# Performance work log

Hardware: AMD Instinct MI355X
Metric: run time of the kernel (lower is better)

## Reference

```python
import jax, jax.numpy as jnp
import numpy as np

N, D, DFF, E, K = 16384, 1024, 4096, 8, 2


def setup_inputs() -> dict:
    key = jax.random.key(0)
    ks = jax.random.split(key, 4)
    return {
        "x": jax.random.normal(ks[0], (N, D), jnp.float32),
        "gate_W": jax.random.normal(ks[1], (D, E), jnp.float32) * (D ** -0.5),
        "gate_b": jnp.zeros((E,), jnp.float32),
        "W1": jax.random.normal(ks[2], (E, D, DFF), jnp.float32) * (D ** -0.5),
        "b1": jnp.zeros((E, DFF), jnp.float32),
        "W2": jax.random.normal(ks[3], (E, DFF, D), jnp.float32) * (DFF ** -0.5),
        "b2": jnp.zeros((E, D), jnp.float32),
    }


def reference(x, gate_W, gate_b, W1, b1, W2, b2):
    n = x.shape[0]
    # --- gating: top-k logits -> softmax over the selected k ---
    logits = x @ gate_W + gate_b                      # [N, E]
    top_v, top_i = jax.lax.top_k(logits, K)           # [N, K]
    w = jax.nn.softmax(top_v, axis=1)                 # [N, K]
    # combine weight per (token, expert); tokens not routed to e get 0,
    # reproducing the masked gather + weighted index_add_ of the original.
    comb = jnp.zeros((n, E), x.dtype).at[jnp.arange(n)[:, None], top_i].add(w)  # [N, E]

    out = jnp.zeros((n, W2.shape[-1]), x.dtype)
    for e in range(E):  # small fixed expert count
        h = jax.nn.gelu(x @ W1[e] + b1[e], approximate=False)  # [N, DFF]
        y = h @ W2[e] + b2[e]                                   # [N, D]
        out = out + comb[:, e:e + 1] * y
    return out, top_i
```

## Files before the change

### kernel.cpp

```cpp
#include <hip/hip_runtime.h>
#include <math.h>

#define N_TOK 16384
#define DIM   1024
#define DFF_  4096
#define NE    8
#define MAXTILES 264
#define MAXSLOTS (MAXTILES*128)

typedef __attribute__((ext_vector_type(8))) __bf16 bf16x8;
typedef __attribute__((ext_vector_type(4))) float  f32x4;
typedef __attribute__((ext_vector_type(8))) unsigned short u16x8;

__device__ __forceinline__ unsigned short f2bf(float f) {
    union { float f; unsigned int u; } v; v.f = f;
    unsigned int u = v.u;
    unsigned int r = (u + 0x7fffu + ((u >> 16) & 1u)) >> 16;
    return (unsigned short)r;
}

__device__ __forceinline__ void gl_lds16(const void* g, void* l) {
    __builtin_amdgcn_global_load_lds(
        (const __attribute__((address_space(1))) void*)g,
        (__attribute__((address_space(3))) void*)l, 16, 0, 0);
}

__global__ __launch_bounds__(256)
void conv_x_kernel(const float* __restrict__ in, unsigned short* __restrict__ outp, int n8) {
    for (int i = blockIdx.x * 256 + threadIdx.x; i < n8; i += gridDim.x * 256) {
        const float4* pp = reinterpret_cast<const float4*>(in + (size_t)i * 8);
        float4 a = pp[0], b = pp[1];
        u16x8 o;
        o[0]=f2bf(a.x); o[1]=f2bf(a.y); o[2]=f2bf(a.z); o[3]=f2bf(a.w);
        o[4]=f2bf(b.x); o[5]=f2bf(b.y); o[6]=f2bf(b.z); o[7]=f2bf(b.w);
        *reinterpret_cast<u16x8*>(outp + (size_t)i * 8) = o;
    }
}

__global__ __launch_bounds__(256)
void transpose_conv(const float* __restrict__ in, unsigned short* __restrict__ outp, int R, int C) {
    __shared__ float tile[32][33];
    size_t mat = (size_t)R * C;
    const float* src = in + (size_t)blockIdx.z * mat;
    unsigned short* dst = outp + (size_t)blockIdx.z * mat;
    int c0 = blockIdx.x * 32, r0 = blockIdx.y * 32;
    int tc = threadIdx.x & 31, tr = threadIdx.x >> 5;
#pragma unroll
    for (int i = 0; i < 4; ++i)
        tile[tr + i*8][tc] = src[(size_t)(r0 + tr + i*8) * C + (c0 + tc)];
    __syncthreads();
#pragma unroll
    for (int i = 0; i < 4; ++i) {
        int a = tr + i*8;
        dst[(size_t)(c0 + a) * R + (r0 + tc)] = f2bf(tile[tc][a]);
    }
}

__global__ __launch_bounds__(256)
void gate_kernel(const float* __restrict__ x, const float* __restrict__ gW,
                 const float* __restrict__ gb, float* __restrict__ outIdx,
                 int* __restrict__ tokE, float* __restrict__ tokW, int* __restrict__ counts) {
    int wave = threadIdx.x >> 6, lane = threadIdx.x & 63;
    int tok = blockIdx.x * 4 + wave;
    const float* xr = x + (size_t)tok * DIM;
    float p[NE];
#pragma unroll
    for (int e = 0; e < NE; ++e) p[e] = 0.f;
    for (int i = lane; i < DIM; i += 64) {
        float xi = xr[i];
        const float* g = gW + (size_t)i * NE;
#pragma unroll
        for (int e = 0; e < NE; ++e) p[e] += xi * g[e];
    }
#pragma unroll
    for (int off = 32; off > 0; off >>= 1) {
#pragma unroll
        for (int e = 0; e < NE; ++e) p[e] += __shfl_xor(p[e], off, 64);
    }
    if (lane == 0) {
        float v0 = -1e30f, v1 = -1e30f; int i0 = 0, i1 = 0;
#pragma unroll
        for (int e = 0; e < NE; ++e) {
            float l = p[e] + gb[e];
            if (l > v0)      { v1 = v0; i1 = i0; v0 = l; i0 = e; }
            else if (l > v1) { v1 = l; i1 = e; }
        }
        float e1 = expf(v1 - v0);
        float inv = 1.0f / (1.0f + e1);
        outIdx[tok*2]   = (float)i0;
        outIdx[tok*2+1] = (float)i1;
        tokE[tok*2] = i0; tokE[tok*2+1] = i1;
        tokW[tok*2] = inv; tokW[tok*2+1] = e1 * inv;
        atomicAdd(&counts[i0], 1);
        atomicAdd(&counts[i1], 1);
    }
}

__global__ void offsets_kernel(const int* __restrict__ counts, int* __restrict__ P,
                               int* __restrict__ tileinfo) {
    if (threadIdx.x == 0 && blockIdx.x == 0) {
        int off = 0, tid = 0;
        for (int e = 0; e < NE; ++e) {
            P[e] = off;
            int c = counts[e];
            int nt = (c + 127) >> 7;
            for (int tt = 0; tt < nt; ++tt) {
                tileinfo[tid*4+0] = e;
                tileinfo[tid*4+1] = off + tt*128;
                int v = c - tt*128; if (v > 128) v = 128;
                tileinfo[tid*4+2] = v;
                tid++;
            }
            off += nt << 7;
        }
        for (; tid < MAXTILES; ++tid) tileinfo[tid*4+0] = -1;
    }
}

__global__ __launch_bounds__(256)
void scatter_kernel(const int* __restrict__ tokE, const float* __restrict__ tokW,
                    const int* __restrict__ P, int* __restrict__ cursor,
                    int* __restrict__ rowlist, float* __restrict__ slotW) {
    int tk = blockIdx.x * 256 + threadIdx.x;
    if (tk >= N_TOK) return;
#pragma unroll
    for (int k = 0; k < 2; ++k) {
        int e = tokE[tk*2 + k];
        int pos = atomicAdd(&cursor[e], 1);
        int slot = P[e] + pos;
        rowlist[slot] = tk;
        slotW[slot]  = tokW[tk*2 + k];
    }
}

__global__ __launch_bounds__(256, 2)
void moe_gemm1(const unsigned short* __restrict__ xb,
               const unsigned short* __restrict__ W1t,
               const float* __restrict__ b1,
               const int* __restrict__ tileinfo,
               const int* __restrict__ rowlist,
               unsigned short* __restrict__ h) {
    int rs = blockIdx.x;
    int e = tileinfo[rs*4];
    if (e < 0) return;
    int base   = tileinfo[rs*4+1];
    int nvalid = tileinfo[rs*4+2];
    int colBlk = blockIdx.y;

    __shared__ unsigned short As[128*64];
    __shared__ unsigned short Bs[128*64];

    int t = threadIdx.x;
    int wave = t >> 6, lane = t & 63;
    int wr = wave >> 1, wc = wave & 1;
    int lr = lane >> 3;
    int lk = (lane & 7) * 8;

    const unsigned short* aSrc[4];
    const unsigned short* bSrc[4];
#pragma unroll
    for (int i = 0; i < 4; ++i) {
        int r = i*32 + wave*8 + lr;
        int tok = (r < nvalid) ? rowlist[base + r] : rowlist[base];
        aSrc[i] = xb + (size_t)tok * DIM + lk;
        int cb = colBlk*128 + r;
        bSrc[i] = W1t + (size_t)e * DFF_ * DIM + (size_t)cb * DIM + lk;
    }

    f32x4 acc[4][4] = {};

    for (int kt = 0; kt < DIM/64; ++kt) {
        __syncthreads();
        int ko = kt * 64;
#pragma unroll
        for (int i = 0; i < 4; ++i) {
            gl_lds16(aSrc[i] + ko, &As[(i*32 + wave*8)*64]);
            gl_lds16(bSrc[i] + ko, &Bs[(i*32 + wave*8)*64]);
        }
        __syncthreads();
#pragma unroll
        for (int kk = 0; kk < 2; ++kk) {
            bf16x8 a[4], b[4];
#pragma unroll
            for (int m = 0; m < 4; ++m)
                a[m] = *reinterpret_cast<const bf16x8*>(&As[(wr*64 + m*16 + (lane&15))*64 + kk*32 + (lane>>4)*8]);
#pragma unroll
            for (int n = 0; n < 4; ++n)
                b[n] = *reinterpret_cast<const bf16x8*>(&Bs[(wc*64 + n*16 + (lane&15))*64 + kk*32 + (lane>>4)*8]);
#pragma unroll
            for (int m = 0; m < 4; ++m)
#pragma unroll
                for (int n = 0; n < 4; ++n)
                    acc[m][n] = __builtin_amdgcn_mfma_f32_16x16x32_bf16(a[m], b[n], acc[m][n], 0, 0, 0);
        }
    }

    float bv[4];
#pragma unroll
    for (int n = 0; n < 4; ++n)
        bv[n] = b1[(size_t)e*DFF_ + colBlk*128 + wc*64 + n*16 + (lane & 15)];
#pragma unroll
    for (int m = 0; m < 4; ++m) {
        int rbase = wr*64 + m*16 + (lane>>4)*4;
#pragma unroll
        for (int j = 0; j < 4; ++j) {
            int row = rbase + j;
            size_t hrow = (size_t)(base + row) * DFF_;
#pragma unroll
            for (int n = 0; n < 4; ++n) {
                int col = colBlk*128 + wc*64 + n*16 + (lane & 15);
                unsigned short val;
                if (row < nvalid) {
                    float v = acc[m][n][j] + bv[n];
                    v = 0.5f * v * (1.0f + erff(v * 0.70710678118654752f));
                    val = f2bf(v);
                } else {
                    val = 0;
                }
                h[hrow + col] = val;
            }
        }
    }
}

__global__ __launch_bounds__(256, 2)
void moe_gemm2(const unsigned short* __restrict__ h,
               const unsigned short* __restrict__ W2t,
               const float* __restrict__ b2,
               const int* __restrict__ tileinfo,
               const int* __restrict__ rowlist,
               const float* __restrict__ slotW,
               float* __restrict__ outp) {
    int rs = blockIdx.x;
    int e = tileinfo[rs*4];
    if (e < 0) return;
    int base   = tileinfo[rs*4+1];
    int nvalid = tileinfo[rs*4+2];
    int colBlk = blockIdx.y;

    __shared__ unsigned short As[128*64];
    __shared__ unsigned short Bs[128*64];

    int t = threadIdx.x;
    int wave = t >> 6, lane = t & 63;
    int wr = wave >> 1, wc = wave & 1;
    int lr = lane >> 3;
    int lk = (lane & 7) * 8;

    const unsigned short* aSrc[4];
    const unsigned short* bSrc[4];
#pragma unroll
    for (int i = 0; i < 4; ++i) {
        int r = i*32 + wave*8 + lr;
        aSrc[i] = h + (size_t)(base + r) * DFF_ + lk;
        int cb = colBlk*128 + r;
        bSrc[i] = W2t + (size_t)e * DIM * DFF_ + (size_t)cb * DFF_ + lk;
    }

    f32x4 acc[4][4] = {};

    for (int kt = 0; kt < DFF_/64; ++kt) {
        __syncthreads();
        int ko = kt * 64;
#pragma unroll
        for (int i = 0; i < 4; ++i) {
            gl_lds16(aSrc[i] + ko, &As[(i*32 + wave*8)*64]);
            gl_lds16(bSrc[i] + ko, &Bs[(i*32 + wave*8)*64]);
        }
        __syncthreads();
#pragma unroll
        for (int kk = 0; kk < 2; ++kk) {
            bf16x8 a[4], b[4];
#pragma unroll
            for (int m = 0; m < 4; ++m)
                a[m] = *reinterpret_cast<const bf16x8*>(&As[(wr*64 + m*16 + (lane&15))*64 + kk*32 + (lane>>4)*8]);
#pragma unroll
            for (int n = 0; n < 4; ++n)
                b[n] = *reinterpret_cast<const bf16x8*>(&Bs[(wc*64 + n*16 + (lane&15))*64 + kk*32 + (lane>>4)*8]);
#pragma unroll
            for (int m = 0; m < 4; ++m)
#pragma unroll
                for (int n = 0; n < 4; ++n)
                    acc[m][n] = __builtin_amdgcn_mfma_f32_16x16x32_bf16(a[m], b[n], acc[m][n], 0, 0, 0);
        }
    }

    float bv[4];
#pragma unroll
    for (int n = 0; n < 4; ++n)
        bv[n] = b2[(size_t)e*DIM + colBlk*128 + wc*64 + n*16 + (lane & 15)];
#pragma unroll
    for (int m = 0; m < 4; ++m) {
        int rbase = wr*64 + m*16 + (lane>>4)*4;
#pragma unroll
        for (int j = 0; j < 4; ++j) {
            int row = rbase + j;
            if (row < nvalid) {
                int tok = rowlist[base + row];
                float w = slotW[base + row];
                size_t orow = (size_t)tok * DIM;
#pragma unroll
                for (int n = 0; n < 4; ++n) {
                    int col = colBlk*128 + wc*64 + n*16 + (lane & 15);
                    atomicAdd(&outp[orow + col], w * (acc[m][n][j] + bv[n]));
                }
            }
        }
    }
}

extern "C" void kernel_launch(void* const* d_in, const int* in_sizes, int n_in,
                              void* d_out, int out_size, void* d_ws, size_t ws_size,
                              hipStream_t stream) {
    const float* x  = (const float*)d_in[0];
    const float* gW = (const float*)d_in[1];
    const float* gb = (const float*)d_in[2];
    const float* W1 = (const float*)d_in[3];
    const float* b1 = (const float*)d_in[4];
    const float* W2 = (const float*)d_in[5];
    const float* b2 = (const float*)d_in[6];
    float* outp = (float*)d_out;

    char* ws = (char*)d_ws;
    size_t off = 0;
    auto alloc = [&](size_t bytes) { void* p = ws + off; off += (bytes + 511) & ~(size_t)511; return p; };
    unsigned short* xb   = (unsigned short*)alloc((size_t)N_TOK * DIM * 2);
    unsigned short* W1t  = (unsigned short*)alloc((size_t)NE * DFF_ * DIM * 2);
    unsigned short* W2t  = (unsigned short*)alloc((size_t)NE * DIM * DFF_ * 2);
    unsigned short* hbuf = (unsigned short*)alloc((size_t)MAXSLOTS * DFF_ * 2);
    int*   rowlist = (int*)alloc(MAXSLOTS * 4);
    float* slotW   = (float*)alloc(MAXSLOTS * 4);
    int*   tokE    = (int*)alloc(N_TOK * 2 * 4);
    float* tokW    = (float*)alloc(N_TOK * 2 * 4);
    int*   meta    = (int*)alloc(8192);
    int* counts   = meta;
    int* cursor   = meta + 8;
    int* Parr     = meta + 16;
    int* tileinfo = meta + 32;

    hipMemsetAsync(meta, 0, 8192, stream);
    hipMemsetAsync(outp, 0, (size_t)N_TOK * DIM * sizeof(float), stream);

    conv_x_kernel<<<2048, 256, 0, stream>>>(x, xb, N_TOK * DIM / 8);
    transpose_conv<<<dim3(DFF_/32, DIM/32, NE), 256, 0, stream>>>(W1, W1t, DIM, DFF_);
    transpose_conv<<<dim3(DIM/32, DFF_/32, NE), 256, 0, stream>>>(W2, W2t, DFF_, DIM);

    gate_kernel<<<N_TOK/4, 256, 0, stream>>>(x, gW, gb, outp + (size_t)N_TOK * DIM,
                                             tokE, tokW, counts);
    offsets_kernel<<<1, 64, 0, stream>>>(counts, Parr, tileinfo);
    scatter_kernel<<<N_TOK/256, 256, 0, stream>>>(tokE, tokW, Parr, cursor, rowlist, slotW);

    moe_gemm1<<<dim3(MAXTILES, DFF_/128), 256, 0, stream>>>(xb, W1t, b1, tileinfo, rowlist, hbuf);
    moe_gemm2<<<dim3(MAXTILES, DIM/128), 256, 0, stream>>>(hbuf, W2t, b2, tileinfo, rowlist, slotW, outp);
}
```

Before: 1.825 ms.

## Replace MoE GEMMs with 256x256-tile double-buffered pipelined MFMA kernel

Replaces the two 128x128 single-buffered expert GEMM kernels with one templated 256x256-tile kernel. It uses 512 threads, 128KB of dynamic LDS with XOR swizzling, and double-buffered global-to-LDS staging interleaved with MFMA phases through explicit waitcnt, barriers and setprio. Expert tiles are now 256 rows and blocks are remapped across experts. The offsets kernel is parallelized and now zero-fills padding slots. The exact erf GELU becomes a tanh approximation using __expf, which trades a little accuracy for cheaper epilogue math. The large tiles raise data reuse and cut the number of load/sync steps, at the cost of more padding waste and probably one block per CU.

```diff
diff --git a/kernel.cpp b/kernel.cpp
--- a/kernel.cpp
+++ b/kernel.cpp
@@ -5,8 +5,8 @@
 #define DIM   1024
 #define DFF_  4096
 #define NE    8
-#define MAXTILES 264
-#define MAXSLOTS (MAXTILES*128)
+#define MAXT2 136
+#define MAXSLOTS2 (MAXT2*256)
 
 typedef __attribute__((ext_vector_type(8))) __bf16 bf16x8;
 typedef __attribute__((ext_vector_type(4))) float  f32x4;
@@ -17,6 +17,13 @@
     unsigned int u = v.u;
     unsigned int r = (u + 0x7fffu + ((u >> 16) & 1u)) >> 16;
     return (unsigned short)r;
+}
+
+__device__ __forceinline__ float gelu_t(float x) {
+    float u = 0.7978845608028654f * (x + 0.044715f * x * x * x);
+    float ex = __expf(2.0f * u);
+    float th = 1.0f - 2.0f / (ex + 1.0f);
+    return 0.5f * x * (1.0f + th);
 }
 
 __device__ __forceinline__ void gl_lds16(const void* g, void* l) {
@@ -96,24 +103,40 @@
     }
 }
 
-__global__ void offsets_kernel(const int* __restrict__ counts, int* __restrict__ P,
-                               int* __restrict__ tileinfo) {
-    if (threadIdx.x == 0 && blockIdx.x == 0) {
-        int off = 0, tid = 0;
+__global__ __launch_bounds__(256)
+void offsets_kernel(const int* __restrict__ counts, int* __restrict__ P,
+                    int* __restrict__ tileinfo, int* __restrict__ rowlist,
+                    float* __restrict__ slotW) {
+    __shared__ int ts[NE+1], cn[NE];
+    int t = threadIdx.x;
+    if (t == 0) {
+        int off = 0;
         for (int e = 0; e < NE; ++e) {
-            P[e] = off;
             int c = counts[e];
-            int nt = (c + 127) >> 7;
-            for (int tt = 0; tt < nt; ++tt) {
-                tileinfo[tid*4+0] = e;
-                tileinfo[tid*4+1] = off + tt*128;
-                int v = c - tt*128; if (v > 128) v = 128;
-                tileinfo[tid*4+2] = v;
-                tid++;
-            }
-            off += nt << 7;
+            cn[e] = c; ts[e] = off; P[e] = off;
+            off += ((c + 255) >> 8) << 8;
         }
-        for (; tid < MAXTILES; ++tid) tileinfo[tid*4+0] = -1;
+        ts[NE] = off;
+    }
+    __syncthreads();
+    int total = ts[NE];
+    for (int ti = t; ti < MAXT2; ti += 256) {
+        int s0 = ti * 256;
+        if (s0 < total) {
+            int e = 0;
+#pragma unroll
+            for (int q = 1; q < NE; ++q) if (s0 >= ts[q]) e = q;
+            int v = cn[e] - (s0 - ts[e]);
+            tileinfo[ti*4+0] = e;
+            tileinfo[ti*4+1] = s0;
+            tileinfo[ti*4+2] = v > 256 ? 256 : v;
+        } else tileinfo[ti*4+0] = -1;
+    }
+    for (int s = t; s < total; s += 256) {
+        int e = 0;
+#pragma unroll
+        for (int q = 1; q < NE; ++q) if (s >= ts[q]) e = q;
+        if (s - ts[e] >= cn[e]) { rowlist[s] = 0; slotW[s] = 0.f; }
     }
 }
 
@@ -133,181 +156,199 @@
     }
 }
 
-__global__ __launch_bounds__(256, 2)
-void moe_gemm1(const unsigned short* __restrict__ xb,
-               const unsigned short* __restrict__ W1t,
-               const float* __restrict__ b1,
-               const int* __restrict__ tileinfo,
-               const int* __restrict__ rowlist,
-               unsigned short* __restrict__ h) {
-    int rs = blockIdx.x;
-    int e = tileinfo[rs*4];
+
+#define BAR()  do { __builtin_amdgcn_s_barrier(); __builtin_amdgcn_sched_barrier(0); } while(0)
+#define LGK0() do { asm volatile("s_waitcnt lgkmcnt(0)" ::: "memory"); __builtin_amdgcn_sched_barrier(0); } while(0)
+#define VMC4() do { asm volatile("s_waitcnt vmcnt(4)" ::: "memory"); __builtin_amdgcn_sched_barrier(0); } while(0)
+#define VMC0() do { asm volatile("s_waitcnt vmcnt(0)" ::: "memory"); __builtin_amdgcn_sched_barrier(0); } while(0)
+
+#define STAGE(MAT, H, KT) do { \
+    char* _d = smem + (((KT)&1)*65536) + ((MAT)*32768) + ((H)*16384) + wave*1024; \
+    _Pragma("unroll") \
+    for (int _j = 0; _j < 2; ++_j) { \
+        const unsigned short* _g = ((MAT) ? Bexp : Amat) + ((MAT) ? boff[H][_j] : aoff[H][_j]) + (KT)*64; \
+        gl_lds16(_g, _d + _j*8192); \
+    } } while(0)
+
+#define LDA(DST, SB, MH) do { \
+    _Pragma("unroll") \
+    for (int _mf = 0; _mf < 4; ++_mf) { \
+        DST[_mf][0] = *(const bf16x8*)((SB) + abase + (MH)*8192 + _mf*2048 + ck0); \
+        DST[_mf][1] = *(const bf16x8*)((SB) + abase + (MH)*8192 + _mf*2048 + ck1); \
+    } } while(0)
+
+#define LDB(DST, SB, NH) do { \
+    _Pragma("unroll") \
+    for (int _nf = 0; _nf < 2; ++_nf) { \
+        DST[_nf][0] = *(const bf16x8*)((SB) + bbase + ((NH)*2+_nf)*2048 + ck0); \
+        DST[_nf][1] = *(const bf16x8*)((SB) + bbase + ((NH)*2+_nf)*2048 + ck1); \
+    } } while(0)
+
+#define MMA(MH, NH, A_, B_) do { \
+    __builtin_amdgcn_s_setprio(1); \
+    _Pragma("unroll") \
+    for (int _ks = 0; _ks < 2; ++_ks) \
+    _Pragma("unroll") \
+    for (int _mf = 0; _mf < 4; ++_mf) \
+    _Pragma("unroll") \
+    for (int _nf = 0; _nf < 2; ++_nf) \
+        acc[(MH)*4+_mf][(NH)*2+_nf] = __builtin_amdgcn_mfma_f32_16x16x32_bf16( \
+            A_[_mf][_ks], B_[_nf][_ks], acc[(MH)*4+_mf][(NH)*2+_nf], 0, 0, 0); \
+    __builtin_amdgcn_s_setprio(0); } while(0)
+
+template<int MODE>
+__global__ __launch_bounds__(512, 2)
+void moe_gemm256(const unsigned short* __restrict__ Amat,
+                 const unsigned short* __restrict__ Bmat,
+                 const float* __restrict__ bias,
+                 const int* __restrict__ tileinfo,
+                 const int* __restrict__ rowlist,
+                 const float* __restrict__ slotW,
+                 unsigned short* __restrict__ hout,
+                 float* __restrict__ outp)
+{
+    constexpr int KD    = (MODE == 1) ? DIM : DFF_;
+    constexpr int ND    = (MODE == 1) ? DFF_ : DIM;
+    constexpr int NKT   = KD / 64;
+    constexpr int NITER = NKT / 2;
+
+    int bx  = blockIdx.x;
+    int per = gridDim.x >> 3;
+    int bxs = (bx & 7) * per + (bx >> 3);
+    int e = tileinfo[bxs*4];
     if (e < 0) return;
-    int base   = tileinfo[rs*4+1];
-    int nvalid = tileinfo[rs*4+2];
+    int base   = tileinfo[bxs*4+1];
+    int nvalid = tileinfo[bxs*4+2];
     int colBlk = blockIdx.y;
 
-    __shared__ unsigned short As[128*64];
-    __shared__ unsigned short Bs[128*64];
-
-    int t = threadIdx.x;
-    int wave = t >> 6, lane = t & 63;
-    int wr = wave >> 1, wc = wave & 1;
-    int lr = lane >> 3;
-    int lk = (lane & 7) * 8;
-
-    const unsigned short* aSrc[4];
-    const unsigned short* bSrc[4];
-#pragma unroll
-    for (int i = 0; i < 4; ++i) {
-        int r = i*32 + wave*8 + lr;
-        int tok = (r < nvalid) ? rowlist[base + r] : rowlist[base];
-        aSrc[i] = xb + (size_t)tok * DIM + lk;
-        int cb = colBlk*128 + r;
-        bSrc[i] = W1t + (size_t)e * DFF_ * DIM + (size_t)cb * DIM + lk;
-    }
-
-    f32x4 acc[4][4] = {};
-
-    for (int kt = 0; kt < DIM/64; ++kt) {
-        __syncthreads();
-        int ko = kt * 64;
-#pragma unroll
-        for (int i = 0; i < 4; ++i) {
-            gl_lds16(aSrc[i] + ko, &As[(i*32 + wave*8)*64]);
-            gl_lds16(bSrc[i] + ko, &Bs[(i*32 + wave*8)*64]);
-        }
-        __syncthreads();
-#pragma unroll
-        for (int kk = 0; kk < 2; ++kk) {
-            bf16x8 a[4], b[4];
-#pragma unroll
-            for (int m = 0; m < 4; ++m)
-                a[m] = *reinterpret_cast<const bf16x8*>(&As[(wr*64 + m*16 + (lane&15))*64 + kk*32 + (lane>>4)*8]);
-#pragma unroll
-            for (int n = 0; n < 4; ++n)
-                b[n] = *reinterpret_cast<const bf16x8*>(&Bs[(wc*64 + n*16 + (lane&15))*64 + kk*32 + (lane>>4)*8]);
-#pragma unroll
-            for (int m = 0; m < 4; ++m)
-#pragma unroll
-                for (int n = 0; n < 4; ++n)
-                    acc[m][n] = __builtin_amdgcn_mfma_f32_16x16x32_bf16(a[m], b[n], acc[m][n], 0, 0, 0);
-        }
-    }
-
-    float bv[4];
+    extern __shared__ char smem[];
+
+    int tid = threadIdx.x;
+    int wave = tid >> 6, lane = tid & 63;
+    int wr = wave >> 2, wc = wave & 3;
+
+    int srow = tid >> 3;
+    int schunk = (tid & 7) ^ (srow & 7);
+    unsigned aoff[2][2], boff[2][2];
+#pragma unroll
+    for (int h = 0; h < 2; ++h)
+#pragma unroll
+    for (int j = 0; j < 2; ++j) {
+        int r = h*128 + j*64 + srow;
+        unsigned arow;
+        if constexpr (MODE == 1) arow = (unsigned)rowlist[base + r] * KD;
+        else                     arow = (unsigned)(base + r) * KD;
+        aoff[h][j] = arow + schunk*8;
+        boff[h][j] = (unsigned)(colBlk*256 + r) * KD + schunk*8;
+    }
+    const unsigned short* Bexp = Bmat + (size_t)e * ND * KD;
+
+    int fr = lane & 15, fq = lane >> 4;
+    int abase = wr*16384 + fr*128;
+    int bbase = 32768 + (wc >> 1)*16384 + (wc & 1)*8192 + fr*128;
+    int ck0 = ((0*4 + fq) ^ (lane & 7)) * 16;
+    int ck1 = ((1*4 + fq) ^ (lane & 7)) * 16;
+
+    f32x4 acc[8][4] = {};
+
+    STAGE(0,0,0); STAGE(0,1,0); STAGE(1,0,0); STAGE(1,1,0);
+    STAGE(0,0,1); STAGE(0,1,1);
+    VMC4();
+    BAR();
+
+    for (int i = 0; i < NITER; ++i) {
+        const int kt1 = 2*i + 1;
+        const bool pf = (i < NITER - 1);
+        char* s0 = smem;
+        char* s1 = smem + 65536;
+        bf16x8 a0[4][2], a1[4][2], b0[2][2], b1[2][2];
+
+        LDA(a0, s0, 0); LDB(b0, s0, 0);
+        STAGE(1,0,kt1);
+        BAR(); LGK0();
+        MMA(0,0,a0,b0);
+        BAR();
+        LDA(a1, s0, 1);
+        STAGE(1,1,kt1);
+        BAR(); LGK0();
+        MMA(1,0,a1,b0);
+        BAR();
+        LDB(b1, s0, 1);
+        if (pf) STAGE(0,0,kt1+1);
+        BAR(); LGK0();
+        MMA(1,1,a1,b1);
+        BAR();
+        if (pf) STAGE(0,1,kt1+1);
+        BAR();
+        MMA(0,1,a0,b1);
+        if (pf) { VMC4(); } else { VMC0(); }
+        BAR();
+
+        LDA(a0, s1, 0); LDB(b0, s1, 0);
+        if (pf) STAGE(1,0,kt1+1);
+        BAR(); LGK0();
+        MMA(0,0,a0,b0);
+        BAR();
+        LDA(a1, s1, 1);
+        if (pf) STAGE(1,1,kt1+1);
+        BAR(); LGK0();
+        MMA(1,0,a1,b0);
+        BAR();
+        LDB(b1, s1, 1);
+        if (pf) STAGE(0,0,kt1+2);
+        BAR(); LGK0();
+        MMA(1,1,a1,b1);
+        BAR();
+        if (pf) STAGE(0,1,kt1+2);
+        BAR();
+        MMA(0,1,a0,b1);
+        if (pf) { VMC4(); } else { VMC0(); }
+        BAR();
+    }
+
+    float bcol[4];
 #pragma unroll
     for (int n = 0; n < 4; ++n)
-        bv[n] = b1[(size_t)e*DFF_ + colBlk*128 + wc*64 + n*16 + (lane & 15)];
-#pragma unroll
-    for (int m = 0; m < 4; ++m) {
-        int rbase = wr*64 + m*16 + (lane>>4)*4;
+        bcol[n] = bias[(size_t)e*ND + colBlk*256 + wc*64 + n*16 + fr];
+
+#pragma unroll
+    for (int m = 0; m < 8; ++m) {
+        int rbase = wr*128 + (m >> 2)*64 + (m & 3)*16 + fq*4;
 #pragma unroll
         for (int j = 0; j < 4; ++j) {
-            int row = rbase + j;
-            size_t hrow = (size_t)(base + row) * DFF_;
-#pragma unroll
-            for (int n = 0; n < 4; ++n) {
-                int col = colBlk*128 + wc*64 + n*16 + (lane & 15);
-                unsigned short val;
-                if (row < nvalid) {
-                    float v = acc[m][n][j] + bv[n];
-                    v = 0.5f * v * (1.0f + erff(v * 0.70710678118654752f));
-                    val = f2bf(v);
-                } else {
-                    val = 0;
+            int grow = rbase + j;
+            if constexpr (MODE == 1) {
+                size_t hrow = (size_t)(base + grow) * ND + colBlk*256;
+#pragma unroll
+                for (int n = 0; n < 4; ++n) {
+                    unsigned short val = 0;
+                    if (grow < nvalid)
+                        val = f2bf(gelu_t(acc[m][n][j] + bcol[n]));
+                    hout[hrow + wc*64 + n*16 + fr] = val;
                 }
-                h[hrow + col] = val;
-            }
-        }
-    }
-}
-
-__global__ __launch_bounds__(256, 2)
-void moe_gemm2(const unsigned short* __restrict__ h,
-               const unsigned short* __restrict__ W2t,
-               const float* __restrict__ b2,
-               const int* __restrict__ tileinfo,
-               const int* __restrict__ rowlist,
-               const float* __restrict__ slotW,
-               float* __restrict__ outp) {
-    int rs = blockIdx.x;
-    int e = tileinfo[rs*4];
-    if (e < 0) return;
-    int base   = tileinfo[rs*4+1];
-    int nvalid = tileinfo[rs*4+2];
-    int colBlk = blockIdx.y;
-
-    __shared__ unsigned short As[128*64];
-    __shared__ unsigned short Bs[128*64];
-
-    int t = threadIdx.x;
-    int wave = t >> 6, lane = t & 63;
-    int wr = wave >> 1, wc = wave & 1;
-    int lr = lane >> 3;
-    int lk = (lane & 7) * 8;
-
-    const unsigned short* aSrc[4];
-    const unsigned short* bSrc[4];
-#pragma unroll
-    for (int i = 0; i < 4; ++i) {
-        int r = i*32 + wave*8 + lr;
-        aSrc[i] = h + (size_t)(base + r) * DFF_ + lk;
-        int cb = colBlk*128 + r;
-        bSrc[i] = W2t + (size_t)e * DIM * DFF_ + (size_t)cb * DFF_ + lk;
-    }
-
-    f32x4 acc[4][4] = {};
-
-    for (int kt = 0; kt < DFF_/64; ++kt) {
-        __syncthreads();
-        int ko = kt * 64;
-#pragma unroll
-        for (int i = 0; i < 4; ++i) {
-            gl_lds16(aSrc[i] + ko, &As[(i*32 + wave*8)*64]);
-            gl_lds16(bSrc[i] + ko, &Bs[(i*32 + wave*8)*64]);
-        }
-        __syncthreads();
-#pragma unroll
-        for (int kk = 0; kk < 2; ++kk) {
-            bf16x8 a[4], b[4];
-#pragma unroll
-            for (int m = 0; m < 4; ++m)
-                a[m] = *reinterpret_cast<const bf16x8*>(&As[(wr*64 + m*16 + (lane&15))*64 + kk*32 + (lane>>4)*8]);
-#pragma unroll
-            for (int n = 0; n < 4; ++n)
-                b[n] = *reinterpret_cast<const bf16x8*>(&Bs[(wc*64 + n*16 + (lane&15))*64 + kk*32 + (lane>>4)*8]);
-#pragma unroll
-            for (int m = 0; m < 4; ++m)
-#pragma unroll
-                for (int n = 0; n < 4; ++n)
-                    acc[m][n] = __builtin_amdgcn_mfma_f32_16x16x32_bf16(a[m], b[n], acc[m][n], 0, 0, 0);
-        }
-    }
-
-    float bv[4];
-#pragma unroll
-    for (int n = 0; n < 4; ++n)
-        bv[n] = b2[(size_t)e*DIM + colBlk*128 + wc*64 + n*16 + (lane & 15)];
-#pragma unroll
-    for (int m = 0; m < 4; ++m) {
-        int rbase = wr*64 + m*16 + (lane>>4)*4;
-#pragma unroll
-        for (int j = 0; j < 4; ++j) {
-            int row = rbase + j;
-            if (row < nvalid) {
-                int tok = rowlist[base + row];
-                float w = slotW[base + row];
-                size_t orow = (size_t)tok * DIM;
-#pragma unroll
-                for (int n = 0; n < 4; ++n) {
-                    int col = colBlk*128 + wc*64 + n*16 + (lane & 15);
-                    atomicAdd(&outp[orow + col], w * (acc[m][n][j] + bv[n]));
+            } else {
+                if (grow < nvalid) {
+                    int tok = rowlist[base + grow];
+                    float w = slotW[base + grow];
+                    size_t orow = (size_t)tok * DIM + colBlk*256;
+#pragma unroll
+                    for (int n = 0; n < 4; ++n)
+                        atomicAdd(outp + orow + wc*64 + n*16 + fr,
+                                  w * (acc[m][n][j] + bcol[n]));
                 }
             }
         }
     }
 }
+
+#undef BAR
+#undef LGK0
+#undef VMC4
+#undef VMC0
+#undef STAGE
+#undef LDA
+#undef LDB
+#undef MMA
 
 extern "C" void kernel_launch(void* const* d_in, const int* in_sizes, int n_in,
                               void* d_out, int out_size, void* d_ws, size_t ws_size,
@@ -327,9 +368,9 @@
     unsigned short* xb   = (unsigned short*)alloc((size_t)N_TOK * DIM * 2);
     unsigned short* W1t  = (unsigned short*)alloc((size_t)NE * DFF_ * DIM * 2);
     unsigned short* W2t  = (unsigned short*)alloc((size_t)NE * DIM * DFF_ * 2);
-    unsigned short* hbuf = (unsigned short*)alloc((size_t)MAXSLOTS * DFF_ * 2);
-    int*   rowlist = (int*)alloc(MAXSLOTS * 4);
-    float* slotW   = (float*)alloc(MAXSLOTS * 4);
+    unsigned short* hbuf = (unsigned short*)alloc((size_t)MAXSLOTS2 * DFF_ * 2);
+    int*   rowlist = (int*)alloc(MAXSLOTS2 * 4);
+    float* slotW   = (float*)alloc(MAXSLOTS2 * 4);
     int*   tokE    = (int*)alloc(N_TOK * 2 * 4);
     float* tokW    = (float*)alloc(N_TOK * 2 * 4);
     int*   meta    = (int*)alloc(8192);
@@ -347,9 +388,16 @@
 
     gate_kernel<<<N_TOK/4, 256, 0, stream>>>(x, gW, gb, outp + (size_t)N_TOK * DIM,
                                              tokE, tokW, counts);
-    offsets_kernel<<<1, 64, 0, stream>>>(counts, Parr, tileinfo);
+    offsets_kernel<<<1, 256, 0, stream>>>(counts, Parr, tileinfo, rowlist, slotW);
     scatter_kernel<<<N_TOK/256, 256, 0, stream>>>(tokE, tokW, Parr, cursor, rowlist, slotW);
 
-    moe_gemm1<<<dim3(MAXTILES, DFF_/128), 256, 0, stream>>>(xb, W1t, b1, tileinfo, rowlist, hbuf);
-    moe_gemm2<<<dim3(MAXTILES, DIM/128), 256, 0, stream>>>(hbuf, W2t, b2, tileinfo, rowlist, slotW, outp);
-}
+    (void)hipFuncSetAttribute((const void*)moe_gemm256<1>,
+                              hipFuncAttributeMaxDynamicSharedMemorySize, 131072);
+    (void)hipFuncSetAttribute((const void*)moe_gemm256<2>,
+                              hipFuncAttributeMaxDynamicSharedMemorySize, 131072);
+
+    moe_gemm256<1><<<dim3(MAXT2, DFF_/256), 512, 131072, stream>>>(
+        xb, W1t, b1, tileinfo, rowlist, slotW, hbuf, nullptr);
+    moe_gemm256<2><<<dim3(MAXT2, DIM/256), 512, 131072, stream>>>(
+        hbuf, W2t, b2, tileinfo, rowlist, slotW, nullptr, outp);
+}
```

Result: slower. 1.958 ms (+7.3%).
